# Kernel tuning notes

Hardware: AMD Instinct MI355X
Metric: run time of the kernel (lower is better)

The kernel has to match this reference:

```python
import jax, jax.numpy as jnp
import numpy as np

B, S, H = 16, 4096, 1024

def setup_inputs() -> dict:
    key = jax.random.key(0)
    k = jax.random.split(key, 6)
    return {
        "query": jax.random.normal(k[0], (B, 1, H), dtype=jnp.float32),
        "proj_key": jax.random.normal(k[1], (B, S, H), dtype=jnp.float32),
        "value": jax.random.normal(k[2], (B, S, 2 * H), dtype=jnp.float32),
        "Wq": jax.random.normal(k[3], (H, H), dtype=jnp.float32) * (1.0 / np.sqrt(H)),
        "we": jax.random.normal(k[4], (H,), dtype=jnp.float32) * (1.0 / np.sqrt(H)),
        "mask": jax.random.randint(k[5], (B, S), 0, 2, dtype=jnp.int32),
    }

def reference(query, proj_key, value, Wq, we, mask):
    # query: [B,1,H]; torch Linear(no bias): y = x @ W^T
    q = jnp.einsum('bqh,oh->bqo', query, Wq)            # [B,1,H]
    e = jnp.tanh(q + proj_key)                          # [B,S,H] (broadcast over S)
    scores = jnp.einsum('bsh,h->bs', e, we)             # energy_layer -> [B,S]
    scores = jnp.where(mask == 0, -jnp.inf, scores)
    alphas = jax.nn.softmax(scores, axis=-1)            # [B,S]
    context = jnp.einsum('bs,bsd->bd', alphas, value)   # bmm([B,1,S],[B,S,2H])
    return context[:, None, :], alphas[:, None, :]
```

## Files before the change

kernel.cpp:

```cpp
#include <hip/hip_runtime.h>
#include <math.h>

#define BATCH 16
#define SEQ   4096
#define HDIM  1024
#define DV    2048
#define NCH   32
#define SCH   (SEQ / NCH)
#define KFT   512

typedef float vf4 __attribute__((ext_vector_type(4)));

__device__ __forceinline__ float tanh_fast(float x) {
    float e = __expf(2.0f * x);
    return 1.0f - 2.0f * __builtin_amdgcn_rcpf(1.0f + e);
}

__device__ __forceinline__ float4 ntload4(const float4* p) {
    vf4 v = __builtin_nontemporal_load((const vf4*)p);
    return make_float4(v.x, v.y, v.z, v.w);
}

__global__ __launch_bounds__(256) void k1_q(const float* __restrict__ query,
                                            const float* __restrict__ Wq,
                                            float* __restrict__ qout) {
    int wave = threadIdx.x >> 6;
    int lane = threadIdx.x & 63;
    int o = blockIdx.x * 4 + wave;
    const float4* wq4 = (const float4*)(Wq + (size_t)o * HDIM);
    float4 w[4];
#pragma unroll
    for (int k = 0; k < 4; ++k) w[k] = wq4[k * 64 + lane];
#pragma unroll
    for (int b = 0; b < BATCH; ++b) {
        const float4* q4 = (const float4*)(query + b * HDIM);
        float acc = 0.f;
#pragma unroll
        for (int k = 0; k < 4; ++k) {
            float4 q = q4[k * 64 + lane];
            acc += w[k].x * q.x + w[k].y * q.y + w[k].z * q.z + w[k].w * q.w;
        }
#pragma unroll
        for (int off = 32; off; off >>= 1) acc += __shfl_down(acc, off, 64);
        if (lane == 0) qout[b * HDIM + o] = acc;
    }
}

__global__ __launch_bounds__(KFT) void kf_fused(const float* __restrict__ pk,
                                                const float* __restrict__ qv,
                                                const float* __restrict__ we,
                                                const int* __restrict__ mask,
                                                const float* __restrict__ value,
                                                float* __restrict__ scores,
                                                float* __restrict__ partial,
                                                float* __restrict__ chunkz) {
    int bid = blockIdx.x;
    int b = bid >> 5;
    int c = bid & (NCH - 1);
    int s0 = c * SCH;
    int t = threadIdx.x;
    int wave = t >> 6;
    int lane = t & 63;

    __shared__ float s_aa[SCH];
    __shared__ int   s_list[SCH];
    __shared__ int   s_off[SCH];
    __shared__ int   s_nact;
    __shared__ float redz[8];

    if (t < 64) {
        int r0 = b * SEQ + s0 + t;
        int p0 = (mask[r0] != 0);
        unsigned long long b0 = __ballot(p0);
        int n0 = __popcll(b0);
        if (p0) {
            s_list[__popcll(b0 & ((1ull << lane) - 1ull))] = t;
        } else {
            scores[r0] = -INFINITY;
        }
        int r1 = b * SEQ + s0 + 64 + t;
        int p1 = (mask[r1] != 0);
        unsigned long long b1 = __ballot(p1);
        if (p1) {
            s_list[n0 + __popcll(b1 & ((1ull << lane) - 1ull))] = 64 + t;
        } else {
            scores[r1] = -INFINITY;
        }
        if (lane == 0) s_nact = n0 + __popcll(b1);
    }

    const float4* q4  = (const float4*)(qv + b * HDIM);
    const float4* we4 = (const float4*)we;
    float4 qr[4], wr[4];
#pragma unroll
    for (int k = 0; k < 4; ++k) {
        qr[k] = q4[k * 64 + lane];
        wr[k] = we4[k * 64 + lane];
    }
    __syncthreads();
    int nact = s_nact;
    if (t < nact) s_off[t] = (s0 + s_list[t]) * (DV / 4);

    int cnt8 = (nact + 7) >> 3;
    int jbeg = wave * cnt8;
    int jend = jbeg + cnt8;
    if (jend > nact) jend = nact;
    for (int j = jbeg; j < jend; ++j) {
        int s = s_list[j];
        int r = b * SEQ + s0 + s;
        const float4* row = (const float4*)(pk + (size_t)r * HDIM);
        float acc = 0.f;
#pragma unroll
        for (int k = 0; k < 4; ++k) {
            float4 p = ntload4(row + k * 64 + lane);
            acc += tanh_fast(p.x + qr[k].x) * wr[k].x;
            acc += tanh_fast(p.y + qr[k].y) * wr[k].y;
            acc += tanh_fast(p.z + qr[k].z) * wr[k].z;
            acc += tanh_fast(p.w + qr[k].w) * wr[k].w;
        }
#pragma unroll
        for (int off = 32; off; off >>= 1) acc += __shfl_down(acc, off, 64);
        if (lane == 0) {
            s_aa[j] = __expf(acc);
            scores[r] = acc;
        }
    }
    __syncthreads();

    const float4* v4 = (const float4*)(value + (size_t)b * SEQ * DV);
    float4 acc0 = make_float4(0.f, 0.f, 0.f, 0.f);
    float4 acc1 = make_float4(0.f, 0.f, 0.f, 0.f);
    float4 acc2 = make_float4(0.f, 0.f, 0.f, 0.f);
    float4 acc3 = make_float4(0.f, 0.f, 0.f, 0.f);
    int j = 0;
    for (; j + 3 < nact; j += 4) {
        int   o0 = s_off[j],     o1 = s_off[j + 1];
        int   o2 = s_off[j + 2], o3 = s_off[j + 3];
        float w0 = s_aa[j],      w1 = s_aa[j + 1];
        float w2 = s_aa[j + 2],  w3 = s_aa[j + 3];
        float4 u0 = ntload4(v4 + o0 + t);
        float4 u1 = ntload4(v4 + o1 + t);
        float4 u2 = ntload4(v4 + o2 + t);
        float4 u3 = ntload4(v4 + o3 + t);
        acc0.x += w0 * u0.x; acc0.y += w0 * u0.y; acc0.z += w0 * u0.z; acc0.w += w0 * u0.w;
        acc1.x += w1 * u1.x; acc1.y += w1 * u1.y; acc1.z += w1 * u1.z; acc1.w += w1 * u1.w;
        acc2.x += w2 * u2.x; acc2.y += w2 * u2.y; acc2.z += w2 * u2.z; acc2.w += w2 * u2.w;
        acc3.x += w3 * u3.x; acc3.y += w3 * u3.y; acc3.z += w3 * u3.z; acc3.w += w3 * u3.w;
    }
    for (; j < nact; ++j) {
        int   o = s_off[j];
        float w = s_aa[j];
        float4 u = ntload4(v4 + o + t);
        acc0.x += w * u.x; acc0.y += w * u.y; acc0.z += w * u.z; acc0.w += w * u.w;
    }
    acc0.x += acc1.x + acc2.x + acc3.x;
    acc0.y += acc1.y + acc2.y + acc3.y;
    acc0.z += acc1.z + acc2.z + acc3.z;
    acc0.w += acc1.w + acc2.w + acc3.w;
    ((float4*)(partial + (size_t)bid * DV))[t] = acc0;

    float zv = (t < nact) ? s_aa[t] : 0.f;
#pragma unroll
    for (int off = 32; off; off >>= 1) zv += __shfl_down(zv, off, 64);
    if (lane == 0) redz[wave] = zv;
    __syncthreads();
    if (t == 0) {
        float z = 0.f;
#pragma unroll
        for (int i = 0; i < 8; ++i) z += redz[i];
        chunkz[bid] = z;
    }
}

__global__ __launch_bounds__(256) void kz_final(const float* __restrict__ scores,
                                                const float* __restrict__ partial,
                                                const float* __restrict__ chunkz,
                                                float* __restrict__ ctx,
                                                float* __restrict__ alphas) {
    int bid = blockIdx.x;
    int b = bid >> 4;
    int q = bid & 15;
    int t = threadIdx.x;

    __shared__ float s_z[NCH];
    __shared__ float s_half[128];

    if (t < NCH) s_z[t] = chunkz[b * NCH + t];
    __syncthreads();

    float Z = 0.f;
#pragma unroll
    for (int i = 0; i < NCH; ++i) Z += s_z[i];
    float inv = 1.0f / Z;

    {
        float sc = scores[(size_t)b * SEQ + q * 256 + t];
        float e = (sc == -INFINITY) ? 0.f : __expf(sc);
        alphas[(size_t)b * SEQ + q * 256 + t] = e * inv;
    }

    int col = q * 128 + (t & 127);
    int half = t >> 7;
    float sum = 0.f;
    const float* pbase = partial + (size_t)b * NCH * DV + col;
#pragma unroll 4
    for (int cc = half * 16; cc < half * 16 + 16; ++cc)
        sum += pbase[(size_t)cc * DV];
    if (half == 1) s_half[t & 127] = sum;
    __syncthreads();
    if (half == 0)
        ctx[(size_t)b * DV + col] = (sum + s_half[t]) * inv;
}

__global__ __launch_bounds__(256) void k2_scores(const float* __restrict__ pk,
                                                 const float* __restrict__ qv,
                                                 const float* __restrict__ we,
                                                 const int* __restrict__ mask,
                                                 float* __restrict__ scores) {
    int wave = threadIdx.x >> 6;
    int lane = threadIdx.x & 63;
    int r = blockIdx.x * 4 + wave;
    int b = r >> 12;
    if (mask[r] == 0) { if (lane == 0) scores[r] = -INFINITY; return; }
    const float4* row = (const float4*)(pk + (size_t)r * HDIM);
    const float4* q4  = (const float4*)(qv + b * HDIM);
    const float4* we4 = (const float4*)we;
    float acc = 0.f;
#pragma unroll
    for (int k = 0; k < 4; ++k) {
        int idx = k * 64 + lane;
        float4 p = row[idx];
        float4 q = q4[idx];
        float4 w = we4[idx];
        acc += tanh_fast(p.x + q.x) * w.x;
        acc += tanh_fast(p.y + q.y) * w.y;
        acc += tanh_fast(p.z + q.z) * w.z;
        acc += tanh_fast(p.w + q.w) * w.w;
    }
#pragma unroll
    for (int off = 32; off; off >>= 1) acc += __shfl_down(acc, off, 64);
    if (lane == 0) scores[r] = acc;
}

__global__ __launch_bounds__(256) void k3_softmax(const float* __restrict__ scores,
                                                  float* __restrict__ alphas) {
    int b = blockIdx.x;
    int t = threadIdx.x;
    const float* sc = scores + b * SEQ;
    float loc[16];
    float m = -INFINITY;
#pragma unroll
    for (int i = 0; i < 16; ++i) { loc[i] = sc[t + i * 256]; m = fmaxf(m, loc[i]); }
#pragma unroll
    for (int off = 32; off; off >>= 1) m = fmaxf(m, __shfl_down(m, off, 64));
    __shared__ float redm[4];
    if ((t & 63) == 0) redm[t >> 6] = m;
    __syncthreads();
    m = fmaxf(fmaxf(redm[0], redm[1]), fmaxf(redm[2], redm[3]));
    float sum = 0.f;
#pragma unroll
    for (int i = 0; i < 16; ++i) {
        loc[i] = (loc[i] == -INFINITY) ? 0.f : __expf(loc[i] - m);
        sum += loc[i];
    }
#pragma unroll
    for (int off = 32; off; off >>= 1) sum += __shfl_down(sum, off, 64);
    __shared__ float reds[4];
    if ((t & 63) == 0) reds[t >> 6] = sum;
    __syncthreads();
    float inv = 1.0f / (reds[0] + reds[1] + reds[2] + reds[3]);
#pragma unroll
    for (int i = 0; i < 16; ++i) alphas[b * SEQ + t + i * 256] = loc[i] * inv;
}

__global__ __launch_bounds__(256) void k4_atomic(const float* __restrict__ value,
                                                 const float* __restrict__ alphas,
                                                 float* __restrict__ ctx) {
    int bid = blockIdx.x;
    int ch = bid & 31;
    int dt = (bid >> 5) & 1;
    int b  = bid >> 6;
    int t  = threadIdx.x;
    const float4* v4 = (const float4*)(value + (size_t)b * SEQ * DV + dt * 1024);
    const float* al = alphas + b * SEQ + ch * 128;
    float4 acc = make_float4(0.f, 0.f, 0.f, 0.f);
    for (int s = 0; s < 128; ++s) {
        float a = al[s];
        if (a != 0.f) {
            float4 v = v4[(size_t)(ch * 128 + s) * (DV / 4) + t];
            acc.x += a * v.x; acc.y += a * v.y; acc.z += a * v.z; acc.w += a * v.w;
        }
    }
    float* dst = ctx + (size_t)b * DV + dt * 1024 + t * 4;
    atomicAdd(dst + 0, acc.x);
    atomicAdd(dst + 1, acc.y);
    atomicAdd(dst + 2, acc.z);
    atomicAdd(dst + 3, acc.w);
}

extern "C" void kernel_launch(void* const* d_in, const int* in_sizes, int n_in,
                              void* d_out, int out_size, void* d_ws, size_t ws_size,
                              hipStream_t stream) {
    const float* query = (const float*)d_in[0];
    const float* pk    = (const float*)d_in[1];
    const float* value = (const float*)d_in[2];
    const float* Wq    = (const float*)d_in[3];
    const float* we    = (const float*)d_in[4];
    const int*   mask  = (const int*)d_in[5];

    float* out    = (float*)d_out;
    float* ctx    = out;
    float* alphas = out + BATCH * DV;

    float* ws      = (float*)d_ws;
    float* qws     = ws;
    float* scores  = ws + BATCH * HDIM;
    float* chunkz  = scores + BATCH * SEQ;
    float* partial = chunkz + BATCH * NCH;

    k1_q<<<HDIM / 4, 256, 0, stream>>>(query, Wq, qws);

    size_t need = (size_t)(BATCH * HDIM + BATCH * SEQ + BATCH * NCH
                           + (size_t)BATCH * NCH * DV) * sizeof(float);
    if (ws_size >= need) {
        kf_fused<<<BATCH * NCH, KFT, 0, stream>>>(pk, qws, we, mask, value,
                                                  scores, partial, chunkz);
        kz_final<<<BATCH * 16, 256, 0, stream>>>(scores, partial, chunkz,
                                                 ctx, alphas);
    } else {
        k2_scores<<<(BATCH * SEQ) / 4, 256, 0, stream>>>(pk, qws, we, mask, scores);
        k3_softmax<<<BATCH, 256, 0, stream>>>(scores, alphas);
        (void)hipMemsetAsync(ctx, 0, (size_t)BATCH * DV * sizeof(float), stream);
        k4_atomic<<<BATCH * 64, 256, 0, stream>>>(value, alphas, ctx);
    }
}
```

Before: 83.53 us.

## Fuse softmax normalization and context reduction into main kernel via last-block counter

Removes the separate kz_final launch. Each kf_fused block bumps an atomic per-batch counter, and the last block to finish for a batch sums the chunk normalizers, scales the stored weights into alphas and reduces the partial context rows. Blocks now store exp(score) weights instead of raw scores, so the finalizer no longer recomputes the exponentials. The trade-off is that the final reduction runs in only 16 blocks at the tail instead of 256, and it needs threadfence/atomic ordering plus a counter reset in k1_q.

New measurement: 291.6 us. 3.49x slower.

```diff
diff --git a/kernel.cpp b/kernel.cpp
--- a/kernel.cpp
+++ b/kernel.cpp
@@ -23,7 +23,9 @@
 
 __global__ __launch_bounds__(256) void k1_q(const float* __restrict__ query,
                                             const float* __restrict__ Wq,
-                                            float* __restrict__ qout) {
+                                            float* __restrict__ qout,
+                                            int* __restrict__ done) {
+    if (blockIdx.x == 0 && threadIdx.x < BATCH) done[threadIdx.x] = 0;
     int wave = threadIdx.x >> 6;
     int lane = threadIdx.x & 63;
     int o = blockIdx.x * 4 + wave;
@@ -51,9 +53,12 @@
                                                 const float* __restrict__ we,
                                                 const int* __restrict__ mask,
                                                 const float* __restrict__ value,
-                                                float* __restrict__ scores,
+                                                float* __restrict__ weights,
                                                 float* __restrict__ partial,
-                                                float* __restrict__ chunkz) {
+                                                float* __restrict__ chunkz,
+                                                int* __restrict__ done,
+                                                float* __restrict__ ctx,
+                                                float* __restrict__ alphas) {
     int bid = blockIdx.x;
     int b = bid >> 5;
     int c = bid & (NCH - 1);
@@ -67,6 +72,7 @@
     __shared__ int   s_off[SCH];
     __shared__ int   s_nact;
     __shared__ float redz[8];
+    __shared__ int   s_last;
 
     if (t < 64) {
         int r0 = b * SEQ + s0 + t;
@@ -76,7 +82,7 @@
         if (p0) {
             s_list[__popcll(b0 & ((1ull << lane) - 1ull))] = t;
         } else {
-            scores[r0] = -INFINITY;
+            weights[r0] = 0.f;
         }
         int r1 = b * SEQ + s0 + 64 + t;
         int p1 = (mask[r1] != 0);
@@ -84,7 +90,7 @@
         if (p1) {
             s_list[n0 + __popcll(b1 & ((1ull << lane) - 1ull))] = 64 + t;
         } else {
-            scores[r1] = -INFINITY;
+            weights[r1] = 0.f;
         }
         if (lane == 0) s_nact = n0 + __popcll(b1);
     }
@@ -121,8 +127,9 @@
 #pragma unroll
         for (int off = 32; off; off >>= 1) acc += __shfl_down(acc, off, 64);
         if (lane == 0) {
-            s_aa[j] = __expf(acc);
-            scores[r] = acc;
+            float w = __expf(acc);
+            s_aa[j] = w;
+            weights[r] = w;
         }
     }
     __syncthreads();
@@ -170,46 +177,41 @@
         for (int i = 0; i < 8; ++i) z += redz[i];
         chunkz[bid] = z;
     }
-}
-
-__global__ __launch_bounds__(256) void kz_final(const float* __restrict__ scores,
-                                                const float* __restrict__ partial,
-                                                const float* __restrict__ chunkz,
-                                                float* __restrict__ ctx,
-                                                float* __restrict__ alphas) {
-    int bid = blockIdx.x;
-    int b = bid >> 4;
-    int q = bid & 15;
-    int t = threadIdx.x;
-
-    __shared__ float s_z[NCH];
-    __shared__ float s_half[128];
-
-    if (t < NCH) s_z[t] = chunkz[b * NCH + t];
-    __syncthreads();
-
+
+    __threadfence();
+    if (t == 0) s_last = (atomicAdd(&done[b], 1) == NCH - 1);
+    __syncthreads();
+    if (!s_last) return;
+    __threadfence();
+
+    if (t < NCH) s_aa[t] = chunkz[b * NCH + t];
+    __syncthreads();
     float Z = 0.f;
 #pragma unroll
-    for (int i = 0; i < NCH; ++i) Z += s_z[i];
+    for (int i = 0; i < NCH; ++i) Z += s_aa[i];
     float inv = 1.0f / Z;
 
     {
-        float sc = scores[(size_t)b * SEQ + q * 256 + t];
-        float e = (sc == -INFINITY) ? 0.f : __expf(sc);
-        alphas[(size_t)b * SEQ + q * 256 + t] = e * inv;
-    }
-
-    int col = q * 128 + (t & 127);
-    int half = t >> 7;
-    float sum = 0.f;
-    const float* pbase = partial + (size_t)b * NCH * DV + col;
+        const float4* w4 = (const float4*)(weights + (size_t)b * SEQ);
+        float4* a4 = (float4*)(alphas + (size_t)b * SEQ);
+#pragma unroll
+        for (int i = 0; i < 2; ++i) {
+            float4 w = w4[t + i * KFT];
+            a4[t + i * KFT] = make_float4(w.x * inv, w.y * inv, w.z * inv, w.w * inv);
+        }
+    }
+
+    {
+        const float4* p4 = (const float4*)(partial + (size_t)b * NCH * DV);
+        float sx = 0.f, sy = 0.f, sz = 0.f, sw = 0.f;
 #pragma unroll 4
-    for (int cc = half * 16; cc < half * 16 + 16; ++cc)
-        sum += pbase[(size_t)cc * DV];
-    if (half == 1) s_half[t & 127] = sum;
-    __syncthreads();
-    if (half == 0)
-        ctx[(size_t)b * DV + col] = (sum + s_half[t]) * inv;
+        for (int cc = 0; cc < NCH; ++cc) {
+            float4 u = p4[(size_t)cc * (DV / 4) + t];
+            sx += u.x; sy += u.y; sz += u.z; sw += u.w;
+        }
+        ((float4*)(ctx + (size_t)b * DV))[t] =
+            make_float4(sx * inv, sy * inv, sz * inv, sw * inv);
+    }
 }
 
 __global__ __launch_bounds__(256) void k2_scores(const float* __restrict__ pk,
@@ -314,22 +316,23 @@
 
     float* ws      = (float*)d_ws;
     float* qws     = ws;
-    float* scores  = ws + BATCH * HDIM;
-    float* chunkz  = scores + BATCH * SEQ;
+    float* weights = ws + BATCH * HDIM;
+    float* chunkz  = weights + BATCH * SEQ;
     float* partial = chunkz + BATCH * NCH;
-
-    k1_q<<<HDIM / 4, 256, 0, stream>>>(query, Wq, qws);
-
-    size_t need = (size_t)(BATCH * HDIM + BATCH * SEQ + BATCH * NCH
-                           + (size_t)BATCH * NCH * DV) * sizeof(float);
+    int*   done    = (int*)(partial + (size_t)BATCH * NCH * DV);
+
+    size_t need = ((size_t)(BATCH * HDIM + BATCH * SEQ + BATCH * NCH
+                            + (size_t)BATCH * NCH * DV) + BATCH) * sizeof(float);
+
+    k1_q<<<HDIM / 4, 256, 0, stream>>>(query, Wq, qws, done);
+
     if (ws_size >= need) {
         kf_fused<<<BATCH * NCH, KFT, 0, stream>>>(pk, qws, we, mask, value,
-                                                  scores, partial, chunkz);
-        kz_final<<<BATCH * 16, 256, 0, stream>>>(scores, partial, chunkz,
-                                                 ctx, alphas);
+                                                  weights, partial, chunkz,
+                                                  done, ctx, alphas);
     } else {
-        k2_scores<<<(BATCH * SEQ) / 4, 256, 0, stream>>>(pk, qws, we, mask, scores);
-        k3_softmax<<<BATCH, 256, 0, stream>>>(scores, alphas);
+        k2_scores<<<(BATCH * SEQ) / 4, 256, 0, stream>>>(pk, qws, we, mask, weights);
+        k3_softmax<<<BATCH, 256, 0, stream>>>(weights, alphas);
         (void)hipMemsetAsync(ctx, 0, (size_t)BATCH * DV * sizeof(float), stream);
         k4_atomic<<<BATCH * 64, 256, 0, stream>>>(value, alphas, ctx);
     }
```
